# Kernel optimization log

Hardware: AMD Instinct MI355X
Metric: run time of the kernel (lower is better)

Reference implementation:

```python
import jax, jax.numpy as jnp
import numpy as np


def conv1x1(x, w, b):
    # x: [B, Cin, H, W], w: [Cout, Cin], b: [Cout]
    return jnp.einsum('oc,bchw->bohw', w, x) + b[None, :, None, None]


def setup_inputs() -> dict:
    key = jax.random.key(0)
    ks = jax.random.split(key, 10)
    B, C, H, W = 8, 256, 64, 64
    C2 = C // 2
    s = 1.0 / np.sqrt(C)
    s2 = 1.0 / np.sqrt(C2)
    return {
        'x1': jax.random.normal(ks[0], (B, C, H, W), jnp.float32),
        'x2': jax.random.normal(ks[1], (B, C, H, W), jnp.float32),
        'w_th': jax.random.uniform(ks[2], (C2, C), jnp.float32, -s, s),
        'b_th': jax.random.uniform(ks[3], (C2,), jnp.float32, -s, s),
        'w_pi': jax.random.uniform(ks[4], (C2, C), jnp.float32, -s, s),
        'b_pi': jax.random.uniform(ks[5], (C2,), jnp.float32, -s, s),
        'w_g': jax.random.uniform(ks[6], (C2, C), jnp.float32, -s, s),
        'b_g': jax.random.uniform(ks[7], (C2,), jnp.float32, -s, s),
        'w_out': jax.random.uniform(ks[8], (C, C2), jnp.float32, -s2, s2),
        'b_out': jax.random.uniform(ks[9], (C,), jnp.float32, -s2, s2),
    }


def reference(x1, x2, w_th, b_th, w_pi, b_pi, w_g, b_g, w_out, b_out):
    B, C, H, W = x1.shape
    HW = H * W
    res = x1
    # 1x1 conv projections -> [B, C2, HW]
    e1 = conv1x1(x1, w_th, b_th).reshape(B, -1, HW)  # theta
    e2 = conv1x1(x2, w_pi, b_pi).reshape(B, -1, HW)  # phi
    # scores: [B, HW, HW]
    f = jnp.einsum('bcq,bck->bqk', e1, e2)
    # GLOBAL softmax over the whole HWxHW matrix per batch element
    f = jax.nn.softmax(f.reshape(B, HW * HW), axis=1).reshape(B, HW, HW)
    g2 = conv1x1(x2, w_g, b_g).reshape(B, -1, HW)  # [B, C2, HW]
    # out = f @ g2^T -> [B, HW, C2] -> [B, C2, H, W]
    out = jnp.einsum('bqk,bck->bcq', f, g2).reshape(B, -1, H, W)
    out = conv1x1(out, w_out, b_out)
    return out + res
```

## Files before the change

kernel.cpp:

```cpp
#include <hip/hip_runtime.h>

typedef unsigned short u16;
typedef unsigned int u32;
typedef short s16x8 __attribute__((ext_vector_type(8)));
typedef float f32x4 __attribute__((ext_vector_type(4)));

#define HWN 4096
#define CC  256
#define C2  128
#define LOG2E 1.4426950408889634f

static __device__ __forceinline__ u16 f2bf(float f) {
    union { float f; u32 u; } c; c.f = f;
    u32 u = c.u;
    u32 r = (u + 0x7fffu + ((u >> 16) & 1u)) >> 16;
    return (u16)r;
}
static __device__ __forceinline__ float bf2f(u16 u) {
    union { u32 u; float f; } c; c.u = ((u32)u) << 16; return c.f;
}
static __device__ __forceinline__ u32 cvtpk(float lo, float hi) {
    u32 d;
    asm("v_cvt_pk_bf16_f32 %0, %1, %2" : "=v"(d) : "v"(lo), "v"(hi));
    return d;
}
#define GLB(p) ((const __attribute__((address_space(1))) void*)(p))
#define LDS(p) ((__attribute__((address_space(3))) void*)(p))

__global__ __launch_bounds__(256) void k_wcvt(
    const float* __restrict__ w_th, const float* __restrict__ w_pi,
    const float* __restrict__ w_g,  const float* __restrict__ w_out,
    u16* __restrict__ wthb, u16* __restrict__ wpib,
    u16* __restrict__ wgb,  u16* __restrict__ woutb)
{
    int i = blockIdx.x * 256 + threadIdx.x;
    wthb[i]  = f2bf(w_th[i] * LOG2E);
    wpib[i]  = f2bf(w_pi[i]);
    wgb[i]   = f2bf(w_g[i]);
    woutb[i] = f2bf(w_out[i]);
}

__device__ __forceinline__ void load_afrag(const float* __restrict__ px, int g, s16x8 a[8]) {
    #pragma unroll
    for (int ks = 0; ks < 8; ++ks) {
        union { s16x8 v; u16 u[8]; } c;
        #pragma unroll
        for (int j = 0; j < 8; ++j)
            c.u[j] = f2bf(px[(size_t)(ks*32 + g*8 + j) * HWN]);
        a[ks] = c.v;
    }
}

__device__ __forceinline__ void proj_gemm(const s16x8 a[8], const u16* __restrict__ wb,
                                          const float* __restrict__ bias, float bscale,
                                          int m16, int g, f32x4 acc[8]) {
    #pragma unroll
    for (int nb = 0; nb < 8; ++nb) {
        float bv = bias[nb*16 + m16] * bscale;
        acc[nb] = (f32x4){bv, bv, bv, bv};
    }
    #pragma unroll
    for (int ks = 0; ks < 8; ++ks) {
        #pragma unroll
        for (int nb = 0; nb < 8; ++nb) {
            s16x8 bb = *(const s16x8*)&wb[(size_t)(nb*16 + m16)*CC + ks*32 + g*8];
            acc[nb] = __builtin_amdgcn_mfma_f32_16x16x32_bf16(a[ks], bb, acc[nb], 0, 0, 0);
        }
    }
}

__global__ __launch_bounds__(256) void k_projM(
    const float* __restrict__ x1, const float* __restrict__ x2,
    const u16* __restrict__ wthb, const float* __restrict__ b_th,
    const u16* __restrict__ wpib, const float* __restrict__ b_pi,
    const u16* __restrict__ wgb,  const float* __restrict__ b_g,
    u16* __restrict__ e1t, u16* __restrict__ e2t, u16* __restrict__ g2t)
{
    __shared__ u16 gs[C2][72];
    const int tid  = threadIdx.x;
    const int b    = blockIdx.x >> 6;
    const int q0   = (blockIdx.x & 63) * 64;
    const int wid  = __builtin_amdgcn_readfirstlane(tid >> 6);
    const int lane = tid & 63;
    const int m16  = lane & 15;
    const int g    = lane >> 4;

    s16x8 a[8];
    f32x4 acc[8];

    const float* px1 = x1 + (size_t)b*CC*HWN + q0 + wid*16 + m16;
    load_afrag(px1, g, a);
    proj_gemm(a, wthb, b_th, LOG2E, m16, g, acc);
    #pragma unroll
    for (int nb = 0; nb < 8; ++nb)
        #pragma unroll
        for (int r = 0; r < 4; ++r)
            e1t[((size_t)b*HWN + q0 + wid*16 + g*4 + r)*C2 + nb*16 + m16] = f2bf(acc[nb][r]);

    const float* px2 = x2 + (size_t)b*CC*HWN + q0 + wid*16 + m16;
    load_afrag(px2, g, a);
    proj_gemm(a, wpib, b_pi, 1.f, m16, g, acc);
    #pragma unroll
    for (int nb = 0; nb < 8; ++nb)
        #pragma unroll
        for (int r = 0; r < 4; ++r) {
            int q   = q0 + wid*16 + g*4 + r;
            int gix = (nb*2 + (m16 >> 3)) ^ (q & 7);
            e2t[((size_t)b*HWN + q)*C2 + gix*8 + (m16 & 7)] = f2bf(acc[nb][r]);
        }

    proj_gemm(a, wgb, b_g, 1.f, m16, g, acc);
    #pragma unroll
    for (int nb = 0; nb < 8; ++nb)
        #pragma unroll
        for (int r = 0; r < 4; ++r)
            gs[nb*16 + m16][wid*16 + g*4 + r] = f2bf(acc[nb][r]);
    __syncthreads();
    u16* gt = g2t + ((size_t)b*64 + (q0 >> 6))*8192;
    #pragma unroll
    for (int r = 0; r < 4; ++r) {
        int idx = r*256 + tid;
        int row = idx >> 3, c8 = idx & 7;
        union { u16 u[8]; int4 v; } o;
        #pragma unroll
        for (int e = 0; e < 8; ++e) {
            int c  = c8*8 + e;
            int cs = c ^ ((row & 7) << 3);
            int kk = cs >> 5, rem = cs & 31;
            int gg = rem >> 3, jj = rem & 7;
            int ko = kk*32 + ((jj >> 2) << 4) + (gg << 2) + (jj & 3);
            o.u[e] = gs[row][ko];
        }
        *(int4*)&gt[row*64 + c8*8] = o.v;
    }
}

__global__ __launch_bounds__(256, 2) void k_flash(
    const u16* __restrict__ e1t, const u16* __restrict__ e2t,
    const u16* __restrict__ g2t,
    u16* __restrict__ outp0, u16* __restrict__ outp1, float* __restrict__ ms)
{
    __shared__ u16 e2s[2][64*128];
    __shared__ u16 g2s[2][128*64];

    const int tid  = threadIdx.x;
    const int bid  = ((blockIdx.x & 7) << 6) | (blockIdx.x >> 3);
    const int b    = bid >> 6;
    const int qb   = (bid >> 1) & 31;
    const int seg  = bid & 1;
    const int q0   = qb * 128;
    const int wid  = __builtin_amdgcn_readfirstlane(tid >> 6);
    const int lane = tid & 63;
    const int m16  = lane & 15;
    const int g    = lane >> 4;
    const int sw16 = (m16 & 7) << 3;

    s16x8 af[2][4];
    #pragma unroll
    for (int h = 0; h < 2; ++h) {
        const u16* p = e1t + ((size_t)b*HWN + q0 + wid*32 + h*16 + m16)*C2 + g*8;
        #pragma unroll
        for (int kc = 0; kc < 4; ++kc) af[h][kc] = *(const s16x8*)(p + kc*32);
    }

    f32x4 acc[2][8];
    #pragma unroll
    for (int h = 0; h < 2; ++h)
        #pragma unroll
        for (int i = 0; i < 8; ++i) acc[h][i] = (f32x4){0.f,0.f,0.f,0.f};
    float m_w = -INFINITY, s_w = 0.f;

    const u16* e2base = e2t + (size_t)b*HWN*C2;
    const u16* g2base = g2t + (size_t)b*64*8192;
    const int  wof    = wid * 2048;
    const int  lof    = lane * 8;

    {
        const u16* eG = e2base + (size_t)(seg*2048)*C2 + wof + lof;
        const u16* gG = g2base + (size_t)(seg*32)*8192 + wof + lof;
        u16* eL = &e2s[0][0] + wof;
        u16* gL = &g2s[0][0] + wof;
        #pragma unroll
        for (int c = 0; c < 4; ++c) {
            __builtin_amdgcn_global_load_lds(GLB(eG + c*512), LDS(eL + c*512), 16, 0, 0);
            __builtin_amdgcn_global_load_lds(GLB(gG + c*512), LDS(gL + c*512), 16, 0, 0);
        }
    }
    __syncthreads();

    for (int it = 0; it < 32; ++it) {
        const int cur = it & 1;
        if (it + 1 < 32) {
            const int k0n = seg*2048 + (it+1)*64;
            const u16* eG = e2base + (size_t)k0n*C2 + wof + lof;
            const u16* gG = g2base + (size_t)(k0n >> 6)*8192 + wof + lof;
            u16* eL = &e2s[cur ^ 1][0] + wof;
            u16* gL = &g2s[cur ^ 1][0] + wof;
            #pragma unroll
            for (int c = 0; c < 4; ++c) {
                __builtin_amdgcn_global_load_lds(GLB(eG + c*512), LDS(eL + c*512), 16, 0, 0);
                __builtin_amdgcn_global_load_lds(GLB(gG + c*512), LDS(gL + c*512), 16, 0, 0);
            }
        }

        f32x4 s[2][4];
        #pragma unroll
        for (int h = 0; h < 2; ++h)
            #pragma unroll
            for (int j = 0; j < 4; ++j) s[h][j] = (f32x4){0.f,0.f,0.f,0.f};
        #pragma unroll
        for (int j = 0; j < 4; ++j) {
            #pragma unroll
            for (int kc = 0; kc < 4; ++kc) {
                s16x8 aa = *(const s16x8*)&e2s[cur][((j*16+m16)*128 + kc*32 + g*8) ^ sw16];
                s[0][j] = __builtin_amdgcn_mfma_f32_16x16x32_bf16(aa, af[0][kc], s[0][j], 0, 0, 0);
                s[1][j] = __builtin_amdgcn_mfma_f32_16x16x32_bf16(aa, af[1][kc], s[1][j], 0, 0, 0);
            }
        }

        float tm = -INFINITY;
        #pragma unroll
        for (int h = 0; h < 2; ++h)
            #pragma unroll
            for (int j = 0; j < 4; ++j)
                #pragma unroll
                for (int r = 0; r < 4; ++r) tm = fmaxf(tm, s[h][j][r]);
        #pragma unroll
        for (int off = 32; off >= 1; off >>= 1) tm = fmaxf(tm, __shfl_xor(tm, off));
        if (tm > m_w + 11.5416f) {
            const float sc = exp2f(m_w - tm);
            s_w *= sc;
            #pragma unroll
            for (int h = 0; h < 2; ++h)
                #pragma unroll
                for (int i = 0; i < 8; ++i) {
                    acc[h][i][0] *= sc; acc[h][i][1] *= sc;
                    acc[h][i][2] *= sc; acc[h][i][3] *= sc;
                }
            m_w = tm;
        }
        float psum = 0.f;
        u32 w[2][4][2];
        #pragma unroll
        for (int h = 0; h < 2; ++h)
            #pragma unroll
            for (int j = 0; j < 4; ++j) {
                float p0 = exp2f(s[h][j][0] - m_w);
                float p1 = exp2f(s[h][j][1] - m_w);
                float p2 = exp2f(s[h][j][2] - m_w);
                float p3 = exp2f(s[h][j][3] - m_w);
                psum += (p0 + p1) + (p2 + p3);
                w[h][j][0] = cvtpk(p0, p1);
                w[h][j][1] = cvtpk(p2, p3);
            }
        s_w += psum;

        s16x8 pa[2][2];
        #pragma unroll
        for (int h = 0; h < 2; ++h)
            #pragma unroll
            for (int kk = 0; kk < 2; ++kk) {
                union { u32 d[4]; s16x8 v; } pf;
                pf.d[0] = w[h][2*kk][0];
                pf.d[1] = w[h][2*kk][1];
                pf.d[2] = w[h][2*kk+1][0];
                pf.d[3] = w[h][2*kk+1][1];
                pa[h][kk] = pf.v;
            }

        #pragma unroll
        for (int kk = 0; kk < 2; ++kk) {
            #pragma unroll
            for (int fc = 0; fc < 8; ++fc) {
                s16x8 gb = *(const s16x8*)&g2s[cur][((fc*16+m16)*64 + kk*32 + g*8) ^ sw16];
                acc[0][fc] = __builtin_amdgcn_mfma_f32_16x16x32_bf16(pa[0][kk], gb, acc[0][fc], 0, 0, 0);
                acc[1][fc] = __builtin_amdgcn_mfma_f32_16x16x32_bf16(pa[1][kk], gb, acc[1][fc], 0, 0, 0);
            }
        }

        __syncthreads();
    }

    #pragma unroll
    for (int off = 32; off >= 1; off >>= 1) s_w += __shfl_xor(s_w, off);
    if (lane == 0) {
        int idx = b*256 + seg*128 + qb*4 + wid;
        ms[idx*2 + 0] = m_w;
        ms[idx*2 + 1] = s_w;
    }
    const float inv_s = 1.f / s_w;
    u16* op = seg ? outp1 : outp0;
    #pragma unroll
    for (int h = 0; h < 2; ++h)
        #pragma unroll
        for (int fc = 0; fc < 8; ++fc)
            #pragma unroll
            for (int r = 0; r < 4; ++r)
                op[((size_t)b*HWN + q0 + wid*32 + h*16 + g*4 + r)*C2 + fc*16 + m16] =
                    f2bf(acc[h][fc][r] * inv_s);
}

__global__ void k_mz(const float* __restrict__ ms, float* __restrict__ mz)
{
    __shared__ float rmax[4], rsum[4];
    const int b = blockIdx.x, tid = threadIdx.x;
    const int lane = tid & 63, wid = tid >> 6;
    float m = ms[((size_t)b*256 + tid)*2 + 0];
    float s = ms[((size_t)b*256 + tid)*2 + 1];
    float mm = m;
    #pragma unroll
    for (int off = 32; off >= 1; off >>= 1) mm = fmaxf(mm, __shfl_xor(mm, off));
    if (lane == 0) rmax[wid] = mm;
    __syncthreads();
    float M = fmaxf(fmaxf(rmax[0], rmax[1]), fmaxf(rmax[2], rmax[3]));
    float z = s * exp2f(m - M);
    #pragma unroll
    for (int off = 32; off >= 1; off >>= 1) z += __shfl_xor(z, off);
    if (lane == 0) rsum[wid] = z;
    __syncthreads();
    if (tid == 0) { mz[b*2] = M; mz[b*2+1] = rsum[0]+rsum[1]+rsum[2]+rsum[3]; }
}

__global__ __launch_bounds__(256) void k_outM(
    const u16* __restrict__ outp0, const u16* __restrict__ outp1,
    const float* __restrict__ ms, const float* __restrict__ mz,
    const u16* __restrict__ woutb, const float* __restrict__ b_out,
    const float* __restrict__ x1, float* __restrict__ out)
{
    const int tid  = threadIdx.x;
    const int b    = blockIdx.x >> 6;
    const int q0   = (blockIdx.x & 63) * 64;
    const int wv   = tid >> 6;
    const int lane = tid & 63;
    const int m16  = lane & 15;
    const int g    = lane >> 4;
    const int q    = q0 + wv*16 + m16;

    const float M    = mz[b*2];
    const float invZ = 1.f / mz[b*2+1];
    const int idx5   = (q0 >> 5) + (wv >> 1);
    const float a0 = ms[(b*256 + idx5)*2+1]       * exp2f(ms[(b*256 + idx5)*2]       - M) * invZ;
    const float a1 = ms[(b*256 + 128 + idx5)*2+1] * exp2f(ms[(b*256 + 128 + idx5)*2] - M) * invZ;

    s16x8 bfr[4];
    #pragma unroll
    for (int ks = 0; ks < 4; ++ks) {
        union { s16x8 v; u16 u[8]; } o0, o1, oc;
        o0.v = *(const s16x8*)&outp0[((size_t)b*HWN + q)*C2 + ks*32 + g*8];
        o1.v = *(const s16x8*)&outp1[((size_t)b*HWN + q)*C2 + ks*32 + g*8];
        #pragma unroll
        for (int j = 0; j < 8; ++j)
            oc.u[j] = f2bf(a0*bf2f(o0.u[j]) + a1*bf2f(o1.u[j]));
        bfr[ks] = oc.v;
    }

    f32x4 acc[16];
    #pragma unroll
    for (int cb = 0; cb < 16; ++cb) acc[cb] = (f32x4){0.f,0.f,0.f,0.f};
    #pragma unroll
    for (int ks = 0; ks < 4; ++ks) {
        #pragma unroll
        for (int cb = 0; cb < 16; ++cb) {
            s16x8 afr = *(const s16x8*)&woutb[(size_t)(cb*16 + m16)*C2 + ks*32 + g*8];
            acc[cb] = __builtin_amdgcn_mfma_f32_16x16x32_bf16(afr, bfr[ks], acc[cb], 0, 0, 0);
        }
    }

    #pragma unroll
    for (int cb = 0; cb < 16; ++cb) {
        f32x4 bb = *(const f32x4*)&b_out[cb*16 + g*4];
        #pragma unroll
        for (int r = 0; r < 4; ++r) {
            int co = cb*16 + g*4 + r;
            size_t o = ((size_t)b*CC + co)*HWN + q;
            out[o] = acc[cb][r] + bb[r] + x1[o];
        }
    }
}

extern "C" void kernel_launch(void* const* d_in, const int* in_sizes, int n_in,
                              void* d_out, int out_size, void* d_ws, size_t ws_size,
                              hipStream_t stream)
{
    const float* x1   = (const float*)d_in[0];
    const float* x2   = (const float*)d_in[1];
    const float* w_th = (const float*)d_in[2];
    const float* b_th = (const float*)d_in[3];
    const float* w_pi = (const float*)d_in[4];
    const float* b_pi = (const float*)d_in[5];
    const float* w_g  = (const float*)d_in[6];
    const float* b_g  = (const float*)d_in[7];
    const float* w_out= (const float*)d_in[8];
    const float* b_out= (const float*)d_in[9];
    float* out = (float*)d_out;

    char* ws = (char*)d_ws;
    u16*   e1t  = (u16*)(ws);
    u16*   e2t  = (u16*)(ws + 8388608);
    u16*   g2t  = (u16*)(ws + 16777216);
    u16*   outp0= (u16*)(ws + 25165824);
    u16*   outp1= (u16*)(ws + 33554432);
    float* ms   = (float*)(ws + 41943040);
    float* mz   = (float*)(ws + 41959424);
    u16*   wthb = (u16*)(ws + 41959488);
    u16*   wpib = (u16*)(ws + 42025024);
    u16*   wgb  = (u16*)(ws + 42090560);
    u16*   woutb= (u16*)(ws + 42156096);

    k_wcvt <<<dim3(128), dim3(256), 0, stream>>>(w_th, w_pi, w_g, w_out, wthb, wpib, wgb, woutb);
    k_projM<<<dim3(512), dim3(256), 0, stream>>>(x1, x2, wthb, b_th, wpib, b_pi, wgb, b_g,
                                                 e1t, e2t, g2t);
    k_flash<<<dim3(512), dim3(256), 0, stream>>>(e1t, e2t, g2t, outp0, outp1, ms);
    k_mz   <<<dim3(8),   dim3(256), 0, stream>>>(ms, mz);
    k_outM <<<dim3(512), dim3(256), 0, stream>>>(outp0, outp1, ms, mz, woutb, b_out, x1, out);
}
```

Measured before the change: 198.0 us.

## Replace double-buffered async LDS loads with single-buffer synchronous staging

The flash attention loop no longer uses double-buffered LDS tiles filled by asynchronous global_load_lds prefetch. Each iteration now loads the e2 and g2 tiles through registers into a single LDS buffer, bracketed by two barriers. This halves LDS usage and simplifies the load path, but it gives up the overlap of the next tile's memory traffic with the current tile's MFMA work. The per-wave max reduction is also rewritten as a pairwise tree to shorten the dependency chain.

Result: no change. 196.4 us (-0.8%).

```diff
diff --git a/kernel.cpp b/kernel.cpp
--- a/kernel.cpp
+++ b/kernel.cpp
@@ -24,8 +24,6 @@
     asm("v_cvt_pk_bf16_f32 %0, %1, %2" : "=v"(d) : "v"(lo), "v"(hi));
     return d;
 }
-#define GLB(p) ((const __attribute__((address_space(1))) void*)(p))
-#define LDS(p) ((__attribute__((address_space(3))) void*)(p))
 
 __global__ __launch_bounds__(256) void k_wcvt(
     const float* __restrict__ w_th, const float* __restrict__ w_pi,
@@ -140,8 +138,8 @@
     const u16* __restrict__ g2t,
     u16* __restrict__ outp0, u16* __restrict__ outp1, float* __restrict__ ms)
 {
-    __shared__ u16 e2s[2][64*128];
-    __shared__ u16 g2s[2][128*64];
+    __shared__ u16 e2s[64*128];
+    __shared__ u16 g2s[128*64];
 
     const int tid  = threadIdx.x;
     const int bid  = ((blockIdx.x & 7) << 6) | (blockIdx.x >> 3);
@@ -172,36 +170,27 @@
 
     const u16* e2base = e2t + (size_t)b*HWN*C2;
     const u16* g2base = g2t + (size_t)b*64*8192;
-    const int  wof    = wid * 2048;
-    const int  lof    = lane * 8;
-
-    {
-        const u16* eG = e2base + (size_t)(seg*2048)*C2 + wof + lof;
-        const u16* gG = g2base + (size_t)(seg*32)*8192 + wof + lof;
-        u16* eL = &e2s[0][0] + wof;
-        u16* gL = &g2s[0][0] + wof;
-        #pragma unroll
-        for (int c = 0; c < 4; ++c) {
-            __builtin_amdgcn_global_load_lds(GLB(eG + c*512), LDS(eL + c*512), 16, 0, 0);
-            __builtin_amdgcn_global_load_lds(GLB(gG + c*512), LDS(gL + c*512), 16, 0, 0);
-        }
-    }
-    __syncthreads();
+    const int er = tid >> 4, ec = tid & 15;
 
     for (int it = 0; it < 32; ++it) {
-        const int cur = it & 1;
-        if (it + 1 < 32) {
-            const int k0n = seg*2048 + (it+1)*64;
-            const u16* eG = e2base + (size_t)k0n*C2 + wof + lof;
-            const u16* gG = g2base + (size_t)(k0n >> 6)*8192 + wof + lof;
-            u16* eL = &e2s[cur ^ 1][0] + wof;
-            u16* gL = &g2s[cur ^ 1][0] + wof;
-            #pragma unroll
-            for (int c = 0; c < 4; ++c) {
-                __builtin_amdgcn_global_load_lds(GLB(eG + c*512), LDS(eL + c*512), 16, 0, 0);
-                __builtin_amdgcn_global_load_lds(GLB(gG + c*512), LDS(gL + c*512), 16, 0, 0);
-            }
-        }
+        const int k0 = seg*2048 + it*64;
+        __syncthreads();
+        #pragma unroll
+        for (int r = 0; r < 4; ++r) {
+            int row = r*16 + er;
+            int4 v = *(const int4*)(e2base + (size_t)(k0 + row)*C2 + ec*8);
+            *(int4*)&e2s[row*128 + ec*8] = v;
+        }
+        {
+            const u16* gt = g2base + (size_t)(k0 >> 6)*8192;
+            #pragma unroll
+            for (int r = 0; r < 4; ++r) {
+                int off = (r*256 + tid)*8;
+                int4 v = *(const int4*)(gt + off);
+                *(int4*)&g2s[off] = v;
+            }
+        }
+        __syncthreads();
 
         f32x4 s[2][4];
         #pragma unroll
@@ -212,7 +201,7 @@
         for (int j = 0; j < 4; ++j) {
             #pragma unroll
             for (int kc = 0; kc < 4; ++kc) {
-                s16x8 aa = *(const s16x8*)&e2s[cur][((j*16+m16)*128 + kc*32 + g*8) ^ sw16];
+                s16x8 aa = *(const s16x8*)&e2s[((j*16+m16)*128 + kc*32 + g*8) ^ sw16];
                 s[0][j] = __builtin_amdgcn_mfma_f32_16x16x32_bf16(aa, af[0][kc], s[0][j], 0, 0, 0);
                 s[1][j] = __builtin_amdgcn_mfma_f32_16x16x32_bf16(aa, af[1][kc], s[1][j], 0, 0, 0);
             }
@@ -222,9 +211,11 @@
         #pragma unroll
         for (int h = 0; h < 2; ++h)
             #pragma unroll
-            for (int j = 0; j < 4; ++j)
-                #pragma unroll
-                for (int r = 0; r < 4; ++r) tm = fmaxf(tm, s[h][j][r]);
+            for (int j = 0; j < 4; ++j) {
+                float t01 = fmaxf(s[h][j][0], s[h][j][1]);
+                float t23 = fmaxf(s[h][j][2], s[h][j][3]);
+                tm = fmaxf(tm, fmaxf(t01, t23));
+            }
         #pragma unroll
         for (int off = 32; off >= 1; off >>= 1) tm = fmaxf(tm, __shfl_xor(tm, off));
         if (tm > m_w + 11.5416f) {
@@ -272,13 +263,11 @@
         for (int kk = 0; kk < 2; ++kk) {
             #pragma unroll
             for (int fc = 0; fc < 8; ++fc) {
-                s16x8 gb = *(const s16x8*)&g2s[cur][((fc*16+m16)*64 + kk*32 + g*8) ^ sw16];
+                s16x8 gb = *(const s16x8*)&g2s[((fc*16+m16)*64 + kk*32 + g*8) ^ sw16];
                 acc[0][fc] = __builtin_amdgcn_mfma_f32_16x16x32_bf16(pa[0][kk], gb, acc[0][fc], 0, 0, 0);
                 acc[1][fc] = __builtin_amdgcn_mfma_f32_16x16x32_bf16(pa[1][kk], gb, acc[1][fc], 0, 0, 0);
             }
         }
-
-        __syncthreads();
     }
 
     #pragma unroll
```
